# Kernel tuning notes

Hardware: AMD Instinct MI355X
Metric: run time of the kernel (lower is better)

The kernel has to match this reference:

```python
import jax, jax.numpy as jnp
import numpy as np


def _sample_plane(plane, coords):
    """torch.nn.functional.grid_sample, mode='bilinear', padding_mode='zeros',
    align_corners=True.  plane: [C,H,W]; coords: [N,2] with (x,y) in [-1,1]
    (x indexes W, y indexes H, as in torch grid convention).  Returns [N,C]."""
    C, H, W = plane.shape
    x = (coords[:, 0] + 1.0) * 0.5 * (W - 1)
    y = (coords[:, 1] + 1.0) * 0.5 * (H - 1)
    x0f = jnp.floor(x); y0f = jnp.floor(y)
    wx = x - x0f; wy = y - y0f

    def corner(yi, xi):
        valid = (xi >= 0) & (xi < W) & (yi >= 0) & (yi < H)
        xc = jnp.clip(xi, 0, W - 1).astype(jnp.int32)
        yc = jnp.clip(yi, 0, H - 1).astype(jnp.int32)
        return plane[:, yc, xc] * valid.astype(plane.dtype)  # [C,N]

    v00 = corner(y0f, x0f)
    v01 = corner(y0f, x0f + 1)
    v10 = corner(y0f + 1, x0f)
    v11 = corner(y0f + 1, x0f + 1)
    out = (v00 * (1 - wx) * (1 - wy) + v01 * wx * (1 - wy)
           + v10 * (1 - wx) * wy + v11 * wx * wy)
    return out.T  # [N,C]


_sample_batched = jax.vmap(_sample_plane)  # [B,C,H,W],[B,N,2] -> [B,N,C]


def setup_inputs() -> dict:
    key = jax.random.key(0)
    ks = jax.random.split(key, 8)
    B, N, C, R = 4, 131072, 32, 256
    triplanes = jax.random.normal(ks[0], (B, 3, C, R, R), jnp.float32) * 0.1
    coordinates = jax.random.uniform(ks[1], (B, N, 3), jnp.float32, -1.0, 1.0)
    # MLP weights ~ frequency_init(30) / first_layer_sine_init scales
    w0 = jax.random.uniform(ks[2], (128, C), jnp.float32, -1.0 / C, 1.0 / C)
    b0 = jnp.zeros((128,), jnp.float32)
    s1 = np.sqrt(6.0 / 128) / 30.0
    w1 = jax.random.uniform(ks[3], (128, 128), jnp.float32, -s1, s1)
    b1 = jnp.zeros((128,), jnp.float32)
    w2 = jax.random.uniform(ks[4], (1, 128), jnp.float32, -s1, s1)
    b2 = jnp.zeros((1,), jnp.float32)
    return {"triplanes": triplanes, "coordinates": coordinates,
            "w0": w0, "b0": b0, "w1": w1, "b1": b1, "w2": w2, "b2": b2}


def reference(triplanes, coordinates, w0, b0, w1, b1, w2, b2):
    # triplanes: [B,3,C,R,R]; coordinates: [B,N,3]
    xy = _sample_batched(triplanes[:, 0], coordinates[..., 0:2])   # (x,y)
    yz = _sample_batched(triplanes[:, 1], coordinates[..., 1:3])   # (y,z)
    xz = _sample_batched(triplanes[:, 2], coordinates[..., 0::2])  # (x,z)
    features = xy * yz * xz  # aggregate_fn == 'prod'; [B,N,C]
    h = jax.nn.relu(jnp.einsum('bnc,hc->bnh', features, w0) + b0)
    h = jax.nn.relu(jnp.einsum('bnh,gh->bng', h, w1) + b1)
    return jnp.einsum('bng,og->bno', h, w2) + b2  # [B,N,1]
```

## Files before the change

kernel.cpp:

```cpp
#include <hip/hip_runtime.h>
#include <hip/hip_bf16.h>
#include <cstddef>

#define RES 256
#define NCH 32
#define NPT 131072
#define NB  4

typedef _Float16 half8 __attribute__((ext_vector_type(8)));
typedef float    f32x4 __attribute__((ext_vector_type(4)));

#define H0_STRIDE 136

__global__ __launch_bounds__(256) void transpose_fp16_kernel(
    const float* __restrict__ in, _Float16* __restrict__ out)
{
    __shared__ float tile[NCH][260];
    const int bp = blockIdx.y;
    const int y  = blockIdx.x;
    const int t  = threadIdx.x;

    const float4* src4 = (const float4*)(in + (size_t)bp * NCH * RES * RES
                                            + (size_t)y * RES);
    const int lane4 = t & 63;
    const int cw    = t >> 6;
    #pragma unroll
    for (int i = 0; i < 8; ++i) {
        const int c = i * 4 + cw;
        const float4 v = src4[(size_t)c * (RES * RES / 4) + lane4];
        *(float4*)&tile[c][lane4 * 4] = v;
    }
    __syncthreads();

    _Float16* dst = out + ((size_t)bp * RES * RES + (size_t)y * RES) * NCH;
    #pragma unroll
    for (int i = 0; i < 4; ++i) {
        const int j  = i * 256 + t;
        const int x  = j >> 2;
        const int cg = j & 3;
        half8 h;
        #pragma unroll
        for (int k = 0; k < 8; ++k)
            h[k] = (_Float16)tile[cg * 8 + k][x];
        *(half8*)&dst[(size_t)x * NCH + cg * 8] = h;
    }
}

__global__ __launch_bounds__(256) void prep_weights(
    const float* __restrict__ w0, const float* __restrict__ w1,
    _Float16* __restrict__ w0h, _Float16* __restrict__ w1h)
{
    const int i = blockIdx.x * 256 + threadIdx.x;
    if (i < 128 * NCH) w0h[i] = (_Float16)(w0[i] * 16.0f);
    if (i < 128 * 128) w1h[i] = (_Float16)w1[i];
}

__global__ __launch_bounds__(256, 4) void sample_kernel(
    const _Float16* __restrict__ planesT,
    const float* __restrict__ coords,
    _Float16* __restrict__ featOut)
{
    const int gid = blockIdx.x * 256 + threadIdx.x;
    const int pt  = gid >> 1;
    const int hf  = gid & 1;
    const int b   = pt >> 17;

    const float cx = coords[(size_t)pt * 3 + 0];
    const float cy = coords[(size_t)pt * 3 + 1];
    const float cz = coords[(size_t)pt * 3 + 2];

    float f[3][16];
    #pragma unroll
    for (int pl = 0; pl < 3; ++pl) {
        const float u = (pl == 0) ? cx : (pl == 1) ? cy : cx;
        const float v = (pl == 0) ? cy : cz;

        const float fx = (u + 1.0f) * 0.5f * (RES - 1);
        const float fy = (v + 1.0f) * 0.5f * (RES - 1);
        const float x0f = floorf(fx), y0f = floorf(fy);
        const float wx = fx - x0f, wy = fy - y0f;
        const int x0 = (int)x0f, y0 = (int)y0f;
        const bool vx1 = (x0 + 1) < RES;
        const bool vy1 = (y0 + 1) < RES;
        const int x1 = vx1 ? x0 + 1 : RES - 1;
        const int y1 = vy1 ? y0 + 1 : RES - 1;

        float w00 = (1.0f - wx) * (1.0f - wy);
        float w01 = wx * (1.0f - wy);
        float w10 = (1.0f - wx) * wy;
        float w11 = wx * wy;
        if (!vx1) { w01 = 0.0f; w11 = 0.0f; }
        if (!vy1) { w10 = 0.0f; w11 = 0.0f; }

        const _Float16* base = planesT
            + ((size_t)(b * 3 + pl) * RES * RES) * NCH + hf * 16;

        const half8* p00 = (const half8*)(base + (size_t)(y0 * RES + x0) * NCH);
        const half8* p01 = (const half8*)(base + (size_t)(y0 * RES + x1) * NCH);
        const half8* p10 = (const half8*)(base + (size_t)(y1 * RES + x0) * NCH);
        const half8* p11 = (const half8*)(base + (size_t)(y1 * RES + x1) * NCH);

        const half8 a00 = p00[0], b00 = p00[1];
        const half8 a01 = p01[0], b01 = p01[1];
        const half8 a10 = p10[0], b10 = p10[1];
        const half8 a11 = p11[0], b11 = p11[1];

        #pragma unroll
        for (int k = 0; k < 8; ++k) {
            f[pl][k] = fmaf((float)a11[k], w11, fmaf((float)a10[k], w10,
                       fmaf((float)a01[k], w01, (float)a00[k] * w00)));
            f[pl][8 + k] = fmaf((float)b11[k], w11, fmaf((float)b10[k], w10,
                           fmaf((float)b01[k], w01, (float)b00[k] * w00)));
        }
    }

    half8 o0, o1;
    #pragma unroll
    for (int k = 0; k < 8; ++k) {
        o0[k] = (_Float16)(f[0][k]     * f[1][k]     * f[2][k]     * 256.0f);
        o1[k] = (_Float16)(f[0][8 + k] * f[1][8 + k] * f[2][8 + k] * 256.0f);
    }
    _Float16* dst = featOut + (size_t)pt * NCH + hf * 16;
    *(half8*)&dst[0] = o0;
    *(half8*)&dst[8] = o1;
}

__global__ __launch_bounds__(256, 4) void gemm_kernel(
    const _Float16* __restrict__ feat,
    const _Float16* __restrict__ w0h,
    const _Float16* __restrict__ w1h,
    const float* __restrict__ b0, const float* __restrict__ b1,
    const float* __restrict__ w2, const float* __restrict__ b2,
    float* __restrict__ out)
{
    __shared__ __align__(16) _Float16 h0LDS[4][32 * H0_STRIDE];

    const int tid  = threadIdx.x;
    const int wv   = tid >> 6;
    const int lane = tid & 63;
    const int l15  = lane & 15;
    const int quad = lane >> 4;

    const int m0 = blockIdx.x * 128 + wv * 32;

    half8 a0[2];
    #pragma unroll
    for (int mt = 0; mt < 2; ++mt)
        a0[mt] = *(const half8*)&feat[(size_t)(m0 + mt * 16 + l15) * NCH + quad * 8];

    f32x4 acc0[2][8];
    #pragma unroll
    for (int mt = 0; mt < 2; ++mt)
        #pragma unroll
        for (int nt = 0; nt < 8; ++nt)
            acc0[mt][nt] = (f32x4){0.f, 0.f, 0.f, 0.f};

    #pragma unroll
    for (int nt = 0; nt < 8; ++nt) {
        const half8 bfr = *(const half8*)&w0h[(nt * 16 + l15) * NCH + quad * 8];
        #pragma unroll
        for (int mt = 0; mt < 2; ++mt)
            acc0[mt][nt] = __builtin_amdgcn_mfma_f32_16x16x32_f16(
                a0[mt], bfr, acc0[mt][nt], 0, 0, 0);
    }

    float b0v[8];
    #pragma unroll
    for (int nt = 0; nt < 8; ++nt) b0v[nt] = b0[nt * 16 + l15] * 4096.0f;

    #pragma unroll
    for (int mt = 0; mt < 2; ++mt)
        #pragma unroll
        for (int nt = 0; nt < 8; ++nt)
            #pragma unroll
            for (int r = 0; r < 4; ++r) {
                const float hval = fmaxf(acc0[mt][nt][r] + b0v[nt], 0.0f);
                h0LDS[wv][(mt * 16 + quad * 4 + r) * H0_STRIDE + nt * 16 + l15]
                    = (_Float16)hval;
            }

    half8 a1[2][4];
    #pragma unroll
    for (int mt = 0; mt < 2; ++mt)
        #pragma unroll
        for (int ks = 0; ks < 4; ++ks)
            a1[mt][ks] = *(const half8*)
                &h0LDS[wv][(mt * 16 + l15) * H0_STRIDE + ks * 32 + quad * 8];

    f32x4 acc1[2][8];
    #pragma unroll
    for (int mt = 0; mt < 2; ++mt)
        #pragma unroll
        for (int nt = 0; nt < 8; ++nt)
            acc1[mt][nt] = (f32x4){0.f, 0.f, 0.f, 0.f};

    #pragma unroll
    for (int nt = 0; nt < 8; ++nt) {
        #pragma unroll
        for (int ks = 0; ks < 4; ++ks) {
            const half8 bfr = *(const half8*)
                &w1h[(nt * 16 + l15) * 128 + ks * 32 + quad * 8];
            #pragma unroll
            for (int mt = 0; mt < 2; ++mt)
                acc1[mt][nt] = __builtin_amdgcn_mfma_f32_16x16x32_f16(
                    a1[mt][ks], bfr, acc1[mt][nt], 0, 0, 0);
        }
    }

    float b1v[8], w2s[8];
    #pragma unroll
    for (int nt = 0; nt < 8; ++nt) {
        b1v[nt] = b1[nt * 16 + l15] * 4096.0f;
        w2s[nt] = w2[nt * 16 + l15] * (1.0f / 4096.0f);
    }

    float part[2][4];
    #pragma unroll
    for (int mt = 0; mt < 2; ++mt)
        #pragma unroll
        for (int r = 0; r < 4; ++r) part[mt][r] = 0.0f;

    #pragma unroll
    for (int mt = 0; mt < 2; ++mt)
        #pragma unroll
        for (int nt = 0; nt < 8; ++nt) {
            const f32x4 A = acc1[mt][nt];
            #pragma unroll
            for (int r = 0; r < 4; ++r)
                part[mt][r] = fmaf(w2s[nt], fmaxf(A[r] + b1v[nt], 0.0f), part[mt][r]);
        }

    #pragma unroll
    for (int mt = 0; mt < 2; ++mt)
        #pragma unroll
        for (int r = 0; r < 4; ++r) {
            float s = part[mt][r];
            s += __shfl_xor(s, 1);
            s += __shfl_xor(s, 2);
            s += __shfl_xor(s, 4);
            s += __shfl_xor(s, 8);
            part[mt][r] = s;
        }

    if (l15 == 0) {
        const float bias2 = b2[0];
        #pragma unroll
        for (int mt = 0; mt < 2; ++mt)
            #pragma unroll
            for (int r = 0; r < 4; ++r)
                out[m0 + mt * 16 + quad * 4 + r] = part[mt][r] + bias2;
    }
}

__global__ __launch_bounds__(256) void fused_fallback(
    const float* __restrict__ planes, const float* __restrict__ coords,
    const float* __restrict__ w0, const float* __restrict__ b0,
    const float* __restrict__ w1, const float* __restrict__ b1,
    const float* __restrict__ w2, const float* __restrict__ b2,
    float* __restrict__ out)
{
    const int t = blockIdx.x * 256 + threadIdx.x;
    const int b = t >> 17;
    const float cx = coords[(size_t)t * 3 + 0];
    const float cy = coords[(size_t)t * 3 + 1];
    const float cz = coords[(size_t)t * 3 + 2];
    float feat[NCH];
    #pragma unroll
    for (int p = 0; p < 3; ++p) {
        const float u = (p == 0) ? cx : (p == 1) ? cy : cx;
        const float v = (p == 0) ? cy : cz;
        const float fx = (u + 1.0f) * 0.5f * (RES - 1);
        const float fy = (v + 1.0f) * 0.5f * (RES - 1);
        const float x0f = floorf(fx), y0f = floorf(fy);
        const float wx = fx - x0f, wy = fy - y0f;
        const int x0 = (int)x0f, y0 = (int)y0f;
        const bool vx1 = (x0 + 1) < RES, vy1 = (y0 + 1) < RES;
        const int x1 = vx1 ? x0 + 1 : RES - 1;
        const int y1 = vy1 ? y0 + 1 : RES - 1;
        float w00 = (1.0f - wx) * (1.0f - wy), w01 = wx * (1.0f - wy);
        float w10 = (1.0f - wx) * wy, w11 = wx * wy;
        if (!vx1) { w01 = 0.0f; w11 = 0.0f; }
        if (!vy1) { w10 = 0.0f; w11 = 0.0f; }
        const float* base = planes + (size_t)(b * 3 + p) * NCH * RES * RES;
        const float* p00 = base + (size_t)y0 * RES + x0;
        const float* p01 = base + (size_t)y0 * RES + x1;
        const float* p10 = base + (size_t)y1 * RES + x0;
        const float* p11 = base + (size_t)y1 * RES + x1;
        #pragma unroll
        for (int c = 0; c < NCH; ++c) {
            const size_t off = (size_t)c * RES * RES;
            float s = p00[off] * w00;
            s = fmaf(p01[off], w01, s);
            s = fmaf(p10[off], w10, s);
            s = fmaf(p11[off], w11, s);
            if (p == 0) feat[c] = s; else feat[c] *= s;
        }
    }
    float h0[128];
    #pragma unroll
    for (int g = 0; g < 128; ++g) {
        const float* wr = w0 + g * NCH;
        float aA = b0[g], aB = 0.0f;
        #pragma unroll
        for (int c = 0; c < NCH; c += 2) {
            aA = fmaf(wr[c], feat[c], aA);
            aB = fmaf(wr[c + 1], feat[c + 1], aB);
        }
        h0[g] = fmaxf(aA + aB, 0.0f);
    }
    float o = b2[0];
    for (int g = 0; g < 128; ++g) {
        const float* wr = w1 + g * 128;
        float aA = b1[g], aB = 0.0f, aC = 0.0f, aD = 0.0f;
        #pragma unroll
        for (int h = 0; h < 128; h += 4) {
            aA = fmaf(wr[h], h0[h], aA);
            aB = fmaf(wr[h + 1], h0[h + 1], aB);
            aC = fmaf(wr[h + 2], h0[h + 2], aC);
            aD = fmaf(wr[h + 3], h0[h + 3], aD);
        }
        o = fmaf(fmaxf((aA + aB) + (aC + aD), 0.0f), w2[g], o);
    }
    out[t] = o;
}

extern "C" void kernel_launch(void* const* d_in, const int* in_sizes, int n_in,
                              void* d_out, int out_size, void* d_ws, size_t ws_size,
                              hipStream_t stream)
{
    const float* trip   = (const float*)d_in[0];
    const float* coords = (const float*)d_in[1];
    const float* w0     = (const float*)d_in[2];
    const float* b0     = (const float*)d_in[3];
    const float* w1     = (const float*)d_in[4];
    const float* b1     = (const float*)d_in[5];
    const float* w2     = (const float*)d_in[6];
    const float* b2     = (const float*)d_in[7];
    float* out = (float*)d_out;

    const size_t planesTBytes = (size_t)NB * 3 * RES * RES * NCH * 2;
    const size_t w0hBytes  = 128 * NCH * 2;
    const size_t w1hBytes  = 128 * 128 * 2;
    const size_t featBytes = (size_t)NB * NPT * NCH * 2;
    const size_t needed = planesTBytes + w0hBytes + w1hBytes + featBytes;

    if (ws_size >= needed) {
        _Float16* planesT = (_Float16*)d_ws;
        _Float16* w0h     = (_Float16*)((char*)d_ws + planesTBytes);
        _Float16* w1h     = (_Float16*)((char*)d_ws + planesTBytes + w0hBytes);
        _Float16* featWS  = (_Float16*)((char*)d_ws + planesTBytes + w0hBytes + w1hBytes);

        transpose_fp16_kernel<<<dim3(RES, NB * 3), 256, 0, stream>>>(trip, planesT);
        prep_weights<<<64, 256, 0, stream>>>(w0, w1, w0h, w1h);
        sample_kernel<<<(NB * NPT * 2) / 256, 256, 0, stream>>>(planesT, coords, featWS);
        gemm_kernel<<<(NB * NPT) / 128, 256, 0, stream>>>(
            featWS, w0h, w1h, b0, b1, w2, b2, out);
    } else {
        fused_fallback<<<(NB * NPT) / 256, 256, 0, stream>>>(
            trip, coords, w0, b0, w1, b1, w2, b2, out);
    }
}
```

Baseline: 329.8 us.

## Cut register pressure: fuse MLP epilogues per N-tile, raise sample occupancy

The gemm kernel now processes each 16-column output tile in a non-unrolled loop. Each tile's bias, ReLU and w2 reduction is applied right after its MFMAs, so the full acc0/acc1 arrays no longer stay live in registers. The sample kernel's launch bounds are raised to 8 waves per SIMD and its feature stores become nontemporal. The intent is to lower VGPR use and raise occupancy to hide gather and memory latency. The cost is less ILP between MFMAs, a possible register spill in the sampler, and nontemporal stores that may bypass cache the gemm kernel would reuse right after.

```diff
diff --git a/kernel.cpp b/kernel.cpp
--- a/kernel.cpp
+++ b/kernel.cpp
@@ -55,7 +55,7 @@
     if (i < 128 * 128) w1h[i] = (_Float16)w1[i];
 }
 
-__global__ __launch_bounds__(256, 4) void sample_kernel(
+__global__ __launch_bounds__(256, 8) void sample_kernel(
     const _Float16* __restrict__ planesT,
     const float* __restrict__ coords,
     _Float16* __restrict__ featOut)
@@ -121,8 +121,8 @@
         o1[k] = (_Float16)(f[0][8 + k] * f[1][8 + k] * f[2][8 + k] * 256.0f);
     }
     _Float16* dst = featOut + (size_t)pt * NCH + hf * 16;
-    *(half8*)&dst[0] = o0;
-    *(half8*)&dst[8] = o1;
+    __builtin_nontemporal_store(o0, (half8*)&dst[0]);
+    __builtin_nontemporal_store(o1, (half8*)&dst[8]);
 }
 
 __global__ __launch_bounds__(256, 4) void gemm_kernel(
@@ -148,36 +148,26 @@
     for (int mt = 0; mt < 2; ++mt)
         a0[mt] = *(const half8*)&feat[(size_t)(m0 + mt * 16 + l15) * NCH + quad * 8];
 
-    f32x4 acc0[2][8];
-    #pragma unroll
-    for (int mt = 0; mt < 2; ++mt)
-        #pragma unroll
-        for (int nt = 0; nt < 8; ++nt)
-            acc0[mt][nt] = (f32x4){0.f, 0.f, 0.f, 0.f};
-
-    #pragma unroll
+    #pragma unroll 1
     for (int nt = 0; nt < 8; ++nt) {
         const half8 bfr = *(const half8*)&w0h[(nt * 16 + l15) * NCH + quad * 8];
+        const float b0g = b0[nt * 16 + l15] * 4096.0f;
+        f32x4 acc[2];
+        #pragma unroll
+        for (int mt = 0; mt < 2; ++mt) {
+            acc[mt] = (f32x4){0.f, 0.f, 0.f, 0.f};
+            acc[mt] = __builtin_amdgcn_mfma_f32_16x16x32_f16(
+                a0[mt], bfr, acc[mt], 0, 0, 0);
+        }
         #pragma unroll
         for (int mt = 0; mt < 2; ++mt)
-            acc0[mt][nt] = __builtin_amdgcn_mfma_f32_16x16x32_f16(
-                a0[mt], bfr, acc0[mt][nt], 0, 0, 0);
-    }
-
-    float b0v[8];
-    #pragma unroll
-    for (int nt = 0; nt < 8; ++nt) b0v[nt] = b0[nt * 16 + l15] * 4096.0f;
-
-    #pragma unroll
-    for (int mt = 0; mt < 2; ++mt)
-        #pragma unroll
-        for (int nt = 0; nt < 8; ++nt)
             #pragma unroll
             for (int r = 0; r < 4; ++r) {
-                const float hval = fmaxf(acc0[mt][nt][r] + b0v[nt], 0.0f);
+                const float hval = fmaxf(acc[mt][r] + b0g, 0.0f);
                 h0LDS[wv][(mt * 16 + quad * 4 + r) * H0_STRIDE + nt * 16 + l15]
                     = (_Float16)hval;
             }
+    }
 
     half8 a1[2][4];
     #pragma unroll
@@ -187,48 +177,34 @@
             a1[mt][ks] = *(const half8*)
                 &h0LDS[wv][(mt * 16 + l15) * H0_STRIDE + ks * 32 + quad * 8];
 
-    f32x4 acc1[2][8];
+    float part[2][4];
     #pragma unroll
     for (int mt = 0; mt < 2; ++mt)
         #pragma unroll
-        for (int nt = 0; nt < 8; ++nt)
-            acc1[mt][nt] = (f32x4){0.f, 0.f, 0.f, 0.f};
-
-    #pragma unroll
+        for (int r = 0; r < 4; ++r) part[mt][r] = 0.0f;
+
+    #pragma unroll 1
     for (int nt = 0; nt < 8; ++nt) {
+        const float b1g = b1[nt * 16 + l15] * 4096.0f;
+        const float w2g = w2[nt * 16 + l15] * (1.0f / 4096.0f);
+        f32x4 acc[2];
+        #pragma unroll
+        for (int mt = 0; mt < 2; ++mt) acc[mt] = (f32x4){0.f, 0.f, 0.f, 0.f};
         #pragma unroll
         for (int ks = 0; ks < 4; ++ks) {
             const half8 bfr = *(const half8*)
                 &w1h[(nt * 16 + l15) * 128 + ks * 32 + quad * 8];
             #pragma unroll
             for (int mt = 0; mt < 2; ++mt)
-                acc1[mt][nt] = __builtin_amdgcn_mfma_f32_16x16x32_f16(
-                    a1[mt][ks], bfr, acc1[mt][nt], 0, 0, 0);
-        }
-    }
-
-    float b1v[8], w2s[8];
-    #pragma unroll
-    for (int nt = 0; nt < 8; ++nt) {
-        b1v[nt] = b1[nt * 16 + l15] * 4096.0f;
-        w2s[nt] = w2[nt * 16 + l15] * (1.0f / 4096.0f);
-    }
-
-    float part[2][4];
-    #pragma unroll
-    for (int mt = 0; mt < 2; ++mt)
-        #pragma unroll
-        for (int r = 0; r < 4; ++r) part[mt][r] = 0.0f;
-
-    #pragma unroll
-    for (int mt = 0; mt < 2; ++mt)
-        #pragma unroll
-        for (int nt = 0; nt < 8; ++nt) {
-            const f32x4 A = acc1[mt][nt];
+                acc[mt] = __builtin_amdgcn_mfma_f32_16x16x32_f16(
+                    a1[mt][ks], bfr, acc[mt], 0, 0, 0);
+        }
+        #pragma unroll
+        for (int mt = 0; mt < 2; ++mt)
             #pragma unroll
             for (int r = 0; r < 4; ++r)
-                part[mt][r] = fmaf(w2s[nt], fmaxf(A[r] + b1v[nt], 0.0f), part[mt][r]);
-        }
+                part[mt][r] = fmaf(w2g, fmaxf(acc[mt][r] + b1g, 0.0f), part[mt][r]);
+    }
 
     #pragma unroll
     for (int mt = 0; mt < 2; ++mt)
```

Result: slower. 534.5 us (+62.1%).
